# Optimization experiments

Hardware: AMD Instinct MI355X
Metric: run time of the kernel (lower is better)

The kernel has to match this reference:

```python
import jax, jax.numpy as jnp
import numpy as np

# shift_direction in the torch module is random.random()>0.5 mapped to {+1,-1};
# we fix it to +1 for determinism.
SHIFT = 1
GROUPS = 2  # the 2688 channels split as (2 groups, 12 channels, 112 height)


def setup_inputs() -> dict:
    key = jax.random.key(0)
    k1, k2 = jax.random.split(key)
    x = jax.random.normal(k1, (1, 24, 112, 112), dtype=jnp.float32)
    W = jax.random.normal(k2, (12, 12, 7), dtype=jnp.float32)  # (in_c, out_c, tap)
    return {"x": x, "W": W}


def reference(x, W):
    # Faithful to: reshape -> unfold(k=(7,1), pad=(3,0)) -> einsum 'loinjm,ikj->loknm'
    # -> reshape (1,24,112,112) -> roll(+1, axis=2).
    # This is a 2-group conv along the width dim with kernel 7, 'same' padding,
    # both groups sharing the SAME (12 -> 12) weight W[i,k,j].
    Wt = jnp.transpose(W, (1, 0, 2))                 # (out_c=12, in_c=12, tap=7)
    kernel = jnp.tile(Wt[:, :, None, :], (GROUPS, 1, 1, 1))  # (24, 12, 1, 7) OIHW
    y = jax.lax.conv_general_dilated(
        x, kernel,
        window_strides=(1, 1),
        padding=((0, 0), (3, 3)),                    # pad only along width
        feature_group_count=GROUPS,
        dimension_numbers=("NCHW", "OIHW", "NCHW"),
    )                                                # (1, 24, 112, 112)
    return jnp.roll(y, SHIFT, axis=2)                # shift along height
```

## Files before the change

kernel.cpp:

```cpp
#include <hip/hip_runtime.h>


__global__ __launch_bounds__(384) void shiftconv_kernel(
    const float* __restrict__ x, const float* __restrict__ W, float* __restrict__ out)
{
    __shared__ float xs[12 * 120];
    __shared__ float ws[12 * 12 * 8];

    const int tid   = threadIdx.x;
    const int h_out = blockIdx.x;
    const int g     = blockIdx.y;
    const int h_src = (h_out + 111) % 112;

    #pragma unroll
    for (int k = 0; k < 3; ++k) {
        int idx = tid + 384 * k;
        int oc  = idx / 96;
        int r   = idx - oc * 96;
        int i   = r >> 3;
        int j   = r & 7;
        ws[idx] = (j < 7) ? W[(i * 12 + oc) * 7 + j] : 0.0f;
    }

    if (tid < 336) {
        int i  = tid / 28;
        int c4 = (tid - i * 28) * 4;
        const float4 v = *reinterpret_cast<const float4*>(
            x + (g * 12 + i) * 12544 + h_src * 112 + c4);
        *reinterpret_cast<float4*>(&xs[i * 120 + 4 + c4]) = v;
    } else if (tid < 360) {
        int z    = tid - 336;
        int row  = z >> 1;
        int side = z & 1;
        *reinterpret_cast<float4*>(&xs[row * 120 + side * 116]) =
            make_float4(0.f, 0.f, 0.f, 0.f);
    }
    __syncthreads();

    if (tid < 336) {
        const int oc     = tid / 28;
        const int k      = tid - oc * 28;
        const int w_base = k * 4;

        float acc0 = 0.f, acc1 = 0.f, acc2 = 0.f, acc3 = 0.f;

        #pragma unroll
        for (int i = 0; i < 12; ++i) {
            const float4 xa = *reinterpret_cast<const float4*>(&xs[i * 120 + w_base]);
            const float4 xb = *reinterpret_cast<const float4*>(&xs[i * 120 + w_base + 4]);
            const float4 xc = *reinterpret_cast<const float4*>(&xs[i * 120 + w_base + 8]);
            const float xv[12] = {xa.x, xa.y, xa.z, xa.w,
                                  xb.x, xb.y, xb.z, xb.w,
                                  xc.x, xc.y, xc.z, xc.w};
            const float4 wa = *reinterpret_cast<const float4*>(&ws[(oc * 12 + i) * 8]);
            const float4 wb = *reinterpret_cast<const float4*>(&ws[(oc * 12 + i) * 8 + 4]);
            const float wv[7] = {wa.x, wa.y, wa.z, wa.w, wb.x, wb.y, wb.z};

            #pragma unroll
            for (int j = 0; j < 7; ++j) {
                acc0 += xv[j + 1] * wv[j];
                acc1 += xv[j + 2] * wv[j];
                acc2 += xv[j + 3] * wv[j];
                acc3 += xv[j + 4] * wv[j];
            }
        }

        *reinterpret_cast<float4*>(out + (g * 12 + oc) * 12544 + h_out * 112 + w_base) =
            make_float4(acc0, acc1, acc2, acc3);
    }
}

extern "C" void kernel_launch(void* const* d_in, const int* in_sizes, int n_in,
                              void* d_out, int out_size, void* d_ws, size_t ws_size,
                              hipStream_t stream) {
    const float* x = (const float*)d_in[0];
    const float* W = (const float*)d_in[1];
    float* out     = (float*)d_out;
    shiftconv_kernel<<<dim3(112, 2), 384, 0, stream>>>(x, W, out);
}
```

Baseline: 59.85 us.

## Drop shared memory staging; map one thread per output quad directly from global

Replaces the per-row block that staged input rows and weights in LDS with a flat grid of 294 blocks of 256 threads. Each thread computes four outputs of one channel by reading its neighbouring input float4s straight from global memory, with edge masking for the padding. Weights are read as scalar loads, with the output channel made wave-uniform through readfirstlane. This removes the LDS fill and barrier, but each input value is now loaded from global (cache) about three times per channel and twelve times across output channels. The readfirstlane assumes every 64-thread wave falls inside one channel, which holds because 3136 is a multiple of 64.

```diff
diff --git a/kernel.cpp b/kernel.cpp
--- a/kernel.cpp
+++ b/kernel.cpp
@@ -1,73 +1,46 @@
 #include <hip/hip_runtime.h>
 
 
-__global__ __launch_bounds__(384) void shiftconv_kernel(
+__global__ __launch_bounds__(256) void shiftconv_kernel(
     const float* __restrict__ x, const float* __restrict__ W, float* __restrict__ out)
 {
-    __shared__ float xs[12 * 120];
-    __shared__ float ws[12 * 12 * 8];
+    const int tid = blockIdx.x * 256 + threadIdx.x;
+    const int c   = tid / 3136;
+    const int rem = tid - c * 3136;
+    const int h   = rem / 28;
+    const int w4  = (rem - h * 28) * 4;
+    const int g   = c / 12;
+    const int oc  = __builtin_amdgcn_readfirstlane(c - g * 12);
+    const int h_src = (h + 111) % 112;
 
-    const int tid   = threadIdx.x;
-    const int h_out = blockIdx.x;
-    const int g     = blockIdx.y;
-    const int h_src = (h_out + 111) % 112;
+    const float* xrow0 = x + (g * 12 * 112 + h_src) * 112;
+
+    float acc0 = 0.f, acc1 = 0.f, acc2 = 0.f, acc3 = 0.f;
 
     #pragma unroll
-    for (int k = 0; k < 3; ++k) {
-        int idx = tid + 384 * k;
-        int oc  = idx / 96;
-        int r   = idx - oc * 96;
-        int i   = r >> 3;
-        int j   = r & 7;
-        ws[idx] = (j < 7) ? W[(i * 12 + oc) * 7 + j] : 0.0f;
+    for (int i = 0; i < 12; ++i) {
+        const float* row = xrow0 + i * 12544;
+        float4 xa = make_float4(0.f, 0.f, 0.f, 0.f);
+        float4 xc = make_float4(0.f, 0.f, 0.f, 0.f);
+        if (w4 > 0)   xa = *reinterpret_cast<const float4*>(row + w4 - 4);
+        const float4 xb = *reinterpret_cast<const float4*>(row + w4);
+        if (w4 < 108) xc = *reinterpret_cast<const float4*>(row + w4 + 4);
+        const float xv[12] = {xa.x, xa.y, xa.z, xa.w,
+                              xb.x, xb.y, xb.z, xb.w,
+                              xc.x, xc.y, xc.z, xc.w};
+        const int wb = (i * 12 + oc) * 7;
+        #pragma unroll
+        for (int j = 0; j < 7; ++j) {
+            const float wj = W[wb + j];
+            acc0 += xv[j + 1] * wj;
+            acc1 += xv[j + 2] * wj;
+            acc2 += xv[j + 3] * wj;
+            acc3 += xv[j + 4] * wj;
+        }
     }
 
-    if (tid < 336) {
-        int i  = tid / 28;
-        int c4 = (tid - i * 28) * 4;
-        const float4 v = *reinterpret_cast<const float4*>(
-            x + (g * 12 + i) * 12544 + h_src * 112 + c4);
-        *reinterpret_cast<float4*>(&xs[i * 120 + 4 + c4]) = v;
-    } else if (tid < 360) {
-        int z    = tid - 336;
-        int row  = z >> 1;
-        int side = z & 1;
-        *reinterpret_cast<float4*>(&xs[row * 120 + side * 116]) =
-            make_float4(0.f, 0.f, 0.f, 0.f);
-    }
-    __syncthreads();
-
-    if (tid < 336) {
-        const int oc     = tid / 28;
-        const int k      = tid - oc * 28;
-        const int w_base = k * 4;
-
-        float acc0 = 0.f, acc1 = 0.f, acc2 = 0.f, acc3 = 0.f;
-
-        #pragma unroll
-        for (int i = 0; i < 12; ++i) {
-            const float4 xa = *reinterpret_cast<const float4*>(&xs[i * 120 + w_base]);
-            const float4 xb = *reinterpret_cast<const float4*>(&xs[i * 120 + w_base + 4]);
-            const float4 xc = *reinterpret_cast<const float4*>(&xs[i * 120 + w_base + 8]);
-            const float xv[12] = {xa.x, xa.y, xa.z, xa.w,
-                                  xb.x, xb.y, xb.z, xb.w,
-                                  xc.x, xc.y, xc.z, xc.w};
-            const float4 wa = *reinterpret_cast<const float4*>(&ws[(oc * 12 + i) * 8]);
-            const float4 wb = *reinterpret_cast<const float4*>(&ws[(oc * 12 + i) * 8 + 4]);
-            const float wv[7] = {wa.x, wa.y, wa.z, wa.w, wb.x, wb.y, wb.z};
-
-            #pragma unroll
-            for (int j = 0; j < 7; ++j) {
-                acc0 += xv[j + 1] * wv[j];
-                acc1 += xv[j + 2] * wv[j];
-                acc2 += xv[j + 3] * wv[j];
-                acc3 += xv[j + 4] * wv[j];
-            }
-        }
-
-        *reinterpret_cast<float4*>(out + (g * 12 + oc) * 12544 + h_out * 112 + w_base) =
-            make_float4(acc0, acc1, acc2, acc3);
-    }
+    *reinterpret_cast<float4*>(out + (c * 112 + h) * 112 + w4) =
+        make_float4(acc0, acc1, acc2, acc3);
 }
 
 extern "C" void kernel_launch(void* const* d_in, const int* in_sizes, int n_in,
@@ -76,5 +49,5 @@
     const float* x = (const float*)d_in[0];
     const float* W = (const float*)d_in[1];
     float* out     = (float*)d_out;
-    shiftconv_kernel<<<dim3(112, 2), 384, 0, stream>>>(x, W, out);
+    shiftconv_kernel<<<294, 256, 0, stream>>>(x, W, out);
 }
```

After: 59.47 us. About the same (-0.6%).
